# Kernel tuning notes

Hardware: AMD Instinct MI355X
Metric: run time of the kernel (lower is better)

The kernel has to match this reference:

```python
import jax, jax.numpy as jnp
import numpy as np

N, E, F, H, C, G = 50000, 800000, 20, 4, 64, 64
D = H * C           # 256 = hidden_dim * heads
OUT = 256
L = 6               # 3 res blocks x depth 2 GATv2 layers
NEG_SLOPE = 0.2     # PyG GATv2Conv default negative_slope


def setup_inputs() -> dict:
    key = jax.random.key(0)
    ks = jax.random.split(key, 16)
    def nrm(k, shape, fan_in):
        return jax.random.normal(k, shape, jnp.float32) * (1.0 / np.sqrt(fan_in))
    return {
        "x": jax.random.normal(ks[0], (N, F), jnp.float32),
        "pos": jax.random.normal(ks[1], (N, 3), jnp.float32) * 10.0,
        "edge_index": jax.random.randint(ks[2], (2, E), 0, N),
        "batch": jnp.sort(jax.random.randint(ks[3], (N,), 0, G)),
        # edge_MLP1 = MLP([1, 32, 1])
        "mlp_w1": nrm(ks[4], (1, 32), 1),
        "mlp_b1": jnp.zeros((32,), jnp.float32),
        "mlp_w2": nrm(ks[5], (32, 1), 32),
        "mlp_b2": jnp.zeros((1,), jnp.float32),
        "w_in": nrm(ks[6], (F, D), F),
        "b_in": jnp.zeros((D,), jnp.float32),
        # 6 stacked GATv2Conv layers (all in=D, heads=H, out-per-head=C)
        "gat_wl": nrm(ks[7], (L, D, D), D),
        "gat_bl": jnp.zeros((L, D), jnp.float32),
        "gat_wr": nrm(ks[8], (L, D, D), D),
        "gat_br": jnp.zeros((L, D), jnp.float32),
        "gat_we": nrm(ks[9], (L, 1, D), 1),      # lin_edge, edge_dim=1, no bias
        "gat_att": nrm(ks[10], (L, H, C), C),
        "gat_bias": jnp.zeros((L, D), jnp.float32),
        # 3 AttentionalAggregation modules: gate_nn=Linear(D,1), nn=Linear(D,D)
        "gate_w": nrm(ks[11], (3, D, 1), D),
        "gate_b": jnp.zeros((3, 1), jnp.float32),
        "nn_w": nrm(ks[12], (3, D, D), D),
        "nn_b": jnp.zeros((3, D), jnp.float32),
        "out_w1": nrm(ks[13], (3 * D, OUT), 3 * D),
        "out_b1": jnp.zeros((OUT,), jnp.float32),
        "out_w2": nrm(ks[14], (OUT, OUT), OUT),
        "out_b2": jnp.zeros((OUT,), jnp.float32),
    }


def _segment_softmax(logits, seg, num_segments):
    m = jax.ops.segment_max(logits, seg, num_segments=num_segments)
    e = jnp.exp(logits - m[seg])
    s = jax.ops.segment_sum(e, seg, num_segments=num_segments)
    return e / (s[seg] + 1e-16)


def _gatv2(h, src, dst, ew, wl, bl, wr, br, we, att, bias):
    # h: [N, D]; ew: [E, 1] edge features
    n = h.shape[0]
    xl = (h @ wl + bl).reshape(n, H, C)           # source-side transform (x_j)
    xr = (h @ wr + br).reshape(n, H, C)           # target-side transform (x_i)
    ee = (ew @ we).reshape(-1, H, C)              # edge transform (no bias)
    xj = xl[src]                                  # [E, H, C]
    g = jax.nn.leaky_relu(xj + xr[dst] + ee, NEG_SLOPE)
    alpha = jnp.einsum('ehc,hc->eh', g, att)      # [E, H]
    alpha = _segment_softmax(alpha, dst, n)       # softmax over incoming edges
    out = jax.ops.segment_sum(xj * alpha[:, :, None], dst, num_segments=n)
    return out.reshape(n, D) + bias


def _agg(h, batch, gw, gb, nw, nb):
    gate = _segment_softmax((h @ gw + gb)[:, 0], batch, G)     # [N]
    v = h @ nw + nb
    return jax.ops.segment_sum(gate[:, None] * v, batch, num_segments=G)


def _forward(x, pos, mlp_w1, mlp_b1, mlp_w2, mlp_b2, w_in, b_in,
             gat_wl, gat_bl, gat_wr, gat_br, gat_we, gat_att, gat_bias,
             gate_w, gate_b, nn_w, nn_b, out_w1, out_b1, out_w2, out_b2,
             edge_index, batch):
    src, dst = edge_index[0], edge_index[1]
    d = jnp.linalg.norm(pos[src] - pos[dst], axis=1)[:, None]          # [E,1]
    ew = jax.nn.relu(jax.nn.relu(d @ mlp_w1 + mlp_b1) @ mlp_w2 + mlp_b2)  # [E,1]
    h = x @ w_in + b_in                                                # [N,D]
    outs = []
    for blk in range(3):
        for j in range(2):
            i = blk * 2 + j
            h = h + _gatv2(h, src, dst, ew, gat_wl[i], gat_bl[i], gat_wr[i],
                           gat_br[i], gat_we[i], gat_att[i], gat_bias[i])
            h = jax.nn.relu(h)   # Dropout -> identity (eval mode)
        outs.append(_agg(h, batch, gate_w[blk], gate_b[blk], nn_w[blk], nn_b[blk]))
    z = jnp.concatenate(outs, axis=1)                                  # [G, 3D]
    enc = jax.nn.relu(z @ out_w1 + out_b1) @ out_w2 + out_b2
    return h, enc


def reference(x, pos, edge_index, batch, mlp_w1, mlp_b1, mlp_w2, mlp_b2,
              w_in, b_in, gat_wl, gat_bl, gat_wr, gat_br, gat_we, gat_att,
              gat_bias, gate_w, gate_b, nn_w, nn_b, out_w1, out_b1,
              out_w2, out_b2):
    return _forward(x, pos, mlp_w1, mlp_b1, mlp_w2, mlp_b2, w_in, b_in,
                    gat_wl, gat_bl, gat_wr, gat_br, gat_we, gat_att, gat_bias,
                    gate_w, gate_b, nn_w, nn_b, out_w1, out_b1, out_w2, out_b2,
                    edge_index, batch)
```

## Files before the change

kernel.cpp:

```cpp
#include <hip/hip_runtime.h>
#include <math.h>

constexpr int F_IN = 20;
constexpr int DDIM = 256;

typedef __attribute__((ext_vector_type(8))) short bf16x8;
typedef __attribute__((ext_vector_type(4))) float f32x4;

__device__ __forceinline__ float lrelu(float x){ return x > 0.f ? x : 0.2f*x; }

__device__ __forceinline__ float b2f(unsigned short u){
  union { unsigned int i; float f; } x; x.i = ((unsigned int)u) << 16; return x.f;
}
__device__ __forceinline__ unsigned short f2b(float f){
  union { float f; unsigned int i; } x; x.f = f;
  unsigned int r = x.i + 0x7fffu + ((x.i >> 16) & 1u);
  return (unsigned short)(r >> 16);
}

__global__ __launch_bounds__(256) void edge_prep_k(
    const int* __restrict__ ei, const float* __restrict__ pos,
    const float* __restrict__ mw1, const float* __restrict__ mb1,
    const float* __restrict__ mw2, const float* __restrict__ mb2,
    float* __restrict__ ew, int* __restrict__ cnt, int E)
{
  int t = blockIdx.x*256 + threadIdx.x;
  if (t >= E) return;
  int s = ei[t], d = ei[E + t];
  float dx = pos[s*3+0]-pos[d*3+0];
  float dy = pos[s*3+1]-pos[d*3+1];
  float dz = pos[s*3+2]-pos[d*3+2];
  float dist = sqrtf(dx*dx+dy*dy+dz*dz);
  float o = mb2[0];
  #pragma unroll
  for (int j=0;j<32;j++){
    float hj = fmaxf(dist*mw1[j]+mb1[j], 0.f);
    o += hj*mw2[j];
  }
  o = fmaxf(o, 0.f);
  ew[t] = o;
  atomicAdd(&cnt[d], 1);
}

__global__ __launch_bounds__(512) void scan1_k(const int* __restrict__ cnt, int* __restrict__ offs,
                                               int* __restrict__ bsum, int n)
{
  __shared__ int t[512];
  int tid = threadIdx.x;
  int i = blockIdx.x*512 + tid;
  int v = (i < n) ? cnt[i] : 0;
  t[tid] = v;
  __syncthreads();
  for (int s = 1; s < 512; s <<= 1) {
    int y = (tid >= s) ? t[tid - s] : 0;
    __syncthreads();
    if (tid >= s) t[tid] += y;
    __syncthreads();
  }
  if (i < n) offs[i] = t[tid] - v;
  if (tid == 511) bsum[blockIdx.x] = t[511];
}

__global__ __launch_bounds__(512) void scan2_k(const int* __restrict__ bsum, int* __restrict__ bpre, int nb)
{
  __shared__ int t[512];
  int tid = threadIdx.x;
  int v = (tid < nb) ? bsum[tid] : 0;
  t[tid] = v;
  __syncthreads();
  for (int s = 1; s < 512; s <<= 1) {
    int y = (tid >= s) ? t[tid - s] : 0;
    __syncthreads();
    if (tid >= s) t[tid] += y;
    __syncthreads();
  }
  bpre[tid] = t[tid] - v;
}

__global__ __launch_bounds__(512) void scan3_k(int* __restrict__ offs, const int* __restrict__ bpre, int n, int e)
{
  int i = blockIdx.x*512 + threadIdx.x;
  if (i < n) offs[i] += bpre[blockIdx.x];
  if (i == 0) offs[n] = e;
}

__global__ __launch_bounds__(256) void scatter_k(const int* __restrict__ ei, const float* __restrict__ ew,
    int* __restrict__ cur, int* __restrict__ ssrc, float* __restrict__ sew, int E)
{
  int t = blockIdx.x*256 + threadIdx.x;
  if (t >= E) return;
  int d = ei[E+t];
  int p = atomicAdd(&cur[d], 1);
  ssrc[p] = ei[t];
  sew[p] = ew[t];
}

__global__ void gseg_k(const int* __restrict__ batch, int* __restrict__ goff, int n){
  int g = threadIdx.x;
  if (g > 64) return;
  int lo = 0, hi = n;
  while (lo < hi){ int mid = (lo + hi) >> 1; if (batch[mid] < g) lo = mid + 1; else hi = mid; }
  goff[g] = lo;
}

__global__ __launch_bounds__(256) void wt_k(const float* __restrict__ gwl, const float* __restrict__ gwr,
                                            unsigned short* __restrict__ Wt)
{
  __shared__ float t[64][65];
  int ct = blockIdx.x;
  int kt = blockIdx.y;
  int layer = blockIdx.z;
  int tid = threadIdx.x;
  int cbase = ct*64, k0 = kt*64;
  const float* src = (cbase < 256) ? (gwl + (size_t)layer*65536) : (gwr + (size_t)layer*65536);
  int csrc0 = (cbase < 256) ? cbase : cbase - 256;
  #pragma unroll
  for (int j = 0; j < 16; ++j){
    int idx = j*256 + tid;
    int kl = idx >> 6, cl = idx & 63;
    t[cl][kl] = src[(size_t)(k0 + kl)*256 + csrc0 + cl];
  }
  __syncthreads();
  #pragma unroll
  for (int j = 0; j < 16; ++j){
    int idx = j*256 + tid;
    int cl = idx >> 6, kl = idx & 63;
    Wt[(size_t)layer*131072 + (size_t)(cbase + cl)*256 + k0 + kl] = f2b(t[cl][kl]);
  }
}

__global__ __launch_bounds__(256) void h0_k(const float* __restrict__ x, const float* __restrict__ w,
    const float* __restrict__ b, float* __restrict__ h, unsigned short* __restrict__ hb, int n)
{
  __shared__ float xs[16][20];
  int row0 = blockIdx.x*16, tid = threadIdx.x;
  for (int idx = tid; idx < 16*20; idx += 256){
    int r = idx/20, c = idx%20;
    int rr = row0 + r;
    xs[r][c] = (rr < n) ? x[rr*20 + c] : 0.f;
  }
  __syncthreads();
  float bj = b[tid];
  float acc[16];
  #pragma unroll
  for (int r=0;r<16;r++) acc[r] = bj;
  for (int k=0;k<20;k++){
    float wv = w[k*256 + tid];
    #pragma unroll
    for (int r=0;r<16;r++) acc[r] += xs[r][k]*wv;
  }
  #pragma unroll
  for (int r=0;r<16;r++){
    int rr = row0 + r;
    if (rr < n){
      h[(size_t)rr*256 + tid] = acc[r];
      hb[(size_t)rr*256 + tid] = f2b(acc[r]);
    }
  }
}

__global__ __launch_bounds__(256) void gemm_mfma_k(
    const unsigned short* __restrict__ hb,
    const unsigned short* __restrict__ Wt,
    const float* __restrict__ bl, const float* __restrict__ br,
    unsigned short* __restrict__ out,
    int n)
{
  __shared__ short As[128*64];
  __shared__ short Bs[128*64];
  int tid = threadIdx.x;
  int lane = tid & 63, wid = tid >> 6;
  int wr = wid >> 1, wc = wid & 1;
  int row0 = blockIdx.x * 128;
  int col0 = blockIdx.y * 128;
  f32x4 acc[4][4] = {};

  for (int k0 = 0; k0 < 256; k0 += 64) {
    #pragma unroll
    for (int j = 0; j < 4; ++j) {
      int c = j*256 + tid;
      int r = c >> 3, q = c & 7;
      int rg = row0 + r; if (rg > n-1) rg = n-1;
      bf16x8 av = *(const bf16x8*)(hb + (size_t)rg*256 + k0 + q*8);
      bf16x8 bv = *(const bf16x8*)(Wt + (size_t)(col0 + r)*256 + k0 + q*8);
      int qs = (q ^ (r & 7)) * 8;
      *(bf16x8*)(As + r*64 + qs) = av;
      *(bf16x8*)(Bs + r*64 + qs) = bv;
    }
    __syncthreads();
    #pragma unroll
    for (int kk = 0; kk < 2; ++kk) {
      bf16x8 a[4], b[4];
      #pragma unroll
      for (int mi = 0; mi < 4; ++mi) {
        int r = wr*64 + mi*16 + (lane & 15);
        int q = (kk*4 + (lane >> 4)) ^ (r & 7);
        a[mi] = *(const bf16x8*)(As + r*64 + q*8);
      }
      #pragma unroll
      for (int ni = 0; ni < 4; ++ni) {
        int r = wc*64 + ni*16 + (lane & 15);
        int q = (kk*4 + (lane >> 4)) ^ (r & 7);
        b[ni] = *(const bf16x8*)(Bs + r*64 + q*8);
      }
      #pragma unroll
      for (int mi = 0; mi < 4; ++mi)
        #pragma unroll
        for (int ni = 0; ni < 4; ++ni)
          acc[mi][ni] = __builtin_amdgcn_mfma_f32_16x16x32_bf16(a[mi], b[ni], acc[mi][ni], 0, 0, 0);
    }
    __syncthreads();
  }

  const float* bias = (col0 < 256) ? bl : br;
  int cb = (col0 < 256) ? col0 : col0 - 256;
  #pragma unroll
  for (int ni = 0; ni < 4; ++ni) {
    int coff = wc*64 + ni*16 + (lane & 15);
    int col = col0 + coff;
    float bv = bias[cb + coff];
    #pragma unroll
    for (int mi = 0; mi < 4; ++mi) {
      #pragma unroll
      for (int e = 0; e < 4; ++e) {
        int row = row0 + wr*64 + mi*16 + (lane >> 4)*4 + e;
        if (row < n) out[(size_t)row*512 + col] = f2b(acc[mi][ni][e] + bv);
      }
    }
  }
}

__global__ __launch_bounds__(256) void gat_agg_k(
    const unsigned short* __restrict__ xlr,
    const int* __restrict__ offs, const int* __restrict__ ssrc, const float* __restrict__ sew,
    const float* __restrict__ we, const float* __restrict__ att, const float* __restrict__ bias,
    float* __restrict__ h, unsigned short* __restrict__ hb, int n)
{
  int wid = blockIdx.x*4 + (threadIdx.x >> 6);
  if (wid >= n) return;
  int lane = threadIdx.x & 63;
  const ushort4* xv = (const ushort4*)xlr;
  ushort4 xru = xv[(size_t)wid*128 + 64 + lane];
  float xrx = b2f(xru.x), xry = b2f(xru.y), xrz = b2f(xru.z), xrw = b2f(xru.w);
  float4 we4 = ((const float4*)we)[lane];
  float4 at4 = ((const float4*)att)[lane];
  float m = -INFINITY, sden = 0.f;
  float ax=0.f, ay=0.f, az=0.f, aw=0.f;
  int k = offs[wid], kend = offs[wid+1];
  int src; float ewv; ushort4 xj;
  if (k < kend){ src = ssrc[k]; ewv = sew[k]; xj = xv[(size_t)src*128 + lane]; }
  while (k < kend){
    float cx = b2f(xj.x), cy = b2f(xj.y), cz = b2f(xj.z), cw = b2f(xj.w);
    float ce = ewv;
    ++k;
    if (k < kend){ src = ssrc[k]; ewv = sew[k]; xj = xv[(size_t)src*128 + lane]; }
    float gx = lrelu(cx + xrx + ce*we4.x);
    float gy = lrelu(cy + xry + ce*we4.y);
    float gz = lrelu(cz + xrz + ce*we4.z);
    float gw_ = lrelu(cw + xrw + ce*we4.w);
    float p = gx*at4.x + gy*at4.y + gz*at4.z + gw_*at4.w;
    p += __shfl_xor(p, 1);
    p += __shfl_xor(p, 2);
    p += __shfl_xor(p, 4);
    p += __shfl_xor(p, 8);
    float mn = fmaxf(m, p);
    float corr = __expf(m - mn);
    float wv = __expf(p - mn);
    sden = sden*corr + wv;
    ax = ax*corr + wv*cx;
    ay = ay*corr + wv*cy;
    az = az*corr + wv*cz;
    aw = aw*corr + wv*cw;
    m = mn;
  }
  float inv = 1.f/(sden + 1e-16f);
  size_t hi = (size_t)wid*64 + lane;
  float4 hv = ((const float4*)h)[hi];
  float4 b4 = ((const float4*)bias)[lane];
  float4 o;
  o.x = fmaxf(hv.x + ax*inv + b4.x, 0.f);
  o.y = fmaxf(hv.y + ay*inv + b4.y, 0.f);
  o.z = fmaxf(hv.z + az*inv + b4.z, 0.f);
  o.w = fmaxf(hv.w + aw*inv + b4.w, 0.f);
  ((float4*)h)[hi] = o;
  ushort4 ob;
  ob.x = f2b(o.x); ob.y = f2b(o.y); ob.z = f2b(o.z); ob.w = f2b(o.w);
  ((ushort4*)hb)[hi] = ob;
}

__global__ __launch_bounds__(256) void logits_k(const float* __restrict__ h, const float* __restrict__ gw,
    const float* __restrict__ gb, float* __restrict__ logit, int n)
{
  int wid = blockIdx.x*4 + (threadIdx.x >> 6);
  if (wid >= n) return;
  int lane = threadIdx.x & 63;
  float4 hv = ((const float4*)h)[(size_t)wid*64 + lane];
  float4 g4 = ((const float4*)gw)[lane];
  float p = hv.x*g4.x + hv.y*g4.y + hv.z*g4.z + hv.w*g4.w;
  #pragma unroll
  for (int s=1; s<64; s<<=1) p += __shfl_xor(p, s);
  if (lane == 0) logit[wid] = p + gb[0];
}

__global__ __launch_bounds__(1024) void pool_k(const float* __restrict__ h, const float* __restrict__ logit,
    const int* __restrict__ goff, float* __restrict__ hbar)
{
  __shared__ float red[1024];
  __shared__ float mS, sS;
  int g = blockIdx.x, tid = threadIdx.x;
  int b0 = goff[g], b1 = goff[g+1];
  float lm = -INFINITY;
  for (int i = b0 + tid; i < b1; i += 1024) lm = fmaxf(lm, logit[i]);
  red[tid] = lm;
  __syncthreads();
  for (int s = 512; s > 0; s >>= 1){
    if (tid < s) red[tid] = fmaxf(red[tid], red[tid+s]);
    __syncthreads();
  }
  if (tid == 0) mS = red[0];
  __syncthreads();
  float m = mS;
  float sw = 0.f;
  for (int i = b0 + tid; i < b1; i += 1024) sw += __expf(logit[i] - m);
  __syncthreads();
  red[tid] = sw;
  __syncthreads();
  for (int s = 512; s > 0; s >>= 1){
    if (tid < s) red[tid] += red[tid+s];
    __syncthreads();
  }
  if (tid == 0) sS = red[0];
  __syncthreads();
  float sden = sS;
  int ch = tid & 255, rs = tid >> 8;
  float acc = 0.f;
  for (int i = b0 + rs; i < b1; i += 4)
    acc += __expf(logit[i] - m) * h[(size_t)i*256 + ch];
  __syncthreads();
  red[tid] = acc;
  __syncthreads();
  if (rs == 0){
    float a = red[ch] + red[256+ch] + red[512+ch] + red[768+ch];
    hbar[g*256 + ch] = a/(sden + 1e-16f);
  }
}

template<int K, bool RELU>
__global__ __launch_bounds__(256) void rowgemm_k(const float* __restrict__ A, const float* __restrict__ W,
    const float* __restrict__ bias, float* __restrict__ out, int ostride)
{
  __shared__ float ar[K];
  int row = blockIdx.x;
  int tid = threadIdx.x;
  for (int i = tid; i < K; i += 256) ar[i] = A[(size_t)row*K + i];
  __syncthreads();
  float acc = bias[tid];
  for (int k = 0; k < K; ++k) acc += ar[k]*W[k*256 + tid];
  if (RELU) acc = fmaxf(acc, 0.f);
  out[(size_t)row*ostride + tid] = acc;
}

extern "C" void kernel_launch(void* const* d_in, const int* in_sizes, int n_in,
                              void* d_out, int out_size, void* d_ws, size_t ws_size,
                              hipStream_t stream)
{
  const float* x     = (const float*)d_in[0];
  const float* pos   = (const float*)d_in[1];
  const int*   ei    = (const int*)d_in[2];
  const int*   batch = (const int*)d_in[3];
  const float* mw1   = (const float*)d_in[4];
  const float* mb1   = (const float*)d_in[5];
  const float* mw2   = (const float*)d_in[6];
  const float* mb2   = (const float*)d_in[7];
  const float* w_in  = (const float*)d_in[8];
  const float* b_in  = (const float*)d_in[9];
  const float* gwl   = (const float*)d_in[10];
  const float* gbl   = (const float*)d_in[11];
  const float* gwr   = (const float*)d_in[12];
  const float* gbr   = (const float*)d_in[13];
  const float* gwe   = (const float*)d_in[14];
  const float* gatt  = (const float*)d_in[15];
  const float* gbias = (const float*)d_in[16];
  const float* gate_w= (const float*)d_in[17];
  const float* gate_b= (const float*)d_in[18];
  const float* nn_w  = (const float*)d_in[19];
  const float* nn_b  = (const float*)d_in[20];
  const float* ow1   = (const float*)d_in[21];
  const float* ob1   = (const float*)d_in[22];
  const float* ow2   = (const float*)d_in[23];
  const float* ob2   = (const float*)d_in[24];

  const int N = in_sizes[0] / F_IN;
  const int E = in_sizes[2] / 2;

  char* ws = (char*)d_ws;
  size_t woff = 0;
  auto alloc = [&](size_t bytes) -> void* {
    void* p = ws + woff;
    woff = (woff + bytes + 255) & ~(size_t)255;
    return p;
  };
  float* ew    = (float*)alloc((size_t)E*4);
  int*   cnt   = (int*)  alloc((size_t)N*4);
  int*   offs  = (int*)  alloc((size_t)(N+1)*4);
  int*   cur   = (int*)  alloc((size_t)N*4);
  int*   bsum  = (int*)  alloc(512*4);
  int*   bpre  = (int*)  alloc(512*4);
  int*   ssrc  = (int*)  alloc((size_t)E*4);
  float* sew   = (float*)alloc((size_t)E*4);
  float* h     = (float*)alloc((size_t)N*DDIM*4);
  unsigned short* hb  = (unsigned short*)alloc((size_t)N*DDIM*2);
  unsigned short* xlr = (unsigned short*)alloc((size_t)N*512*2);
  unsigned short* Wt  = (unsigned short*)alloc((size_t)6*512*256*2);
  float* logit = (float*)alloc((size_t)N*4);
  int*   goff  = (int*)  alloc(68*4);
  float* hbar  = (float*)alloc(64*DDIM*4);
  float* zcat  = (float*)alloc(64*768*4);
  float* t1    = (float*)alloc(64*DDIM*4);
  (void)ws_size; (void)n_in; (void)out_size;

  hipMemsetAsync(cnt, 0, (size_t)N*4, stream);

  int eb = (E + 255)/256;
  edge_prep_k<<<eb, 256, 0, stream>>>(ei, pos, mw1, mb1, mw2, mb2, ew, cnt, E);
  int nb = (N + 511)/512;
  scan1_k<<<nb, 512, 0, stream>>>(cnt, offs, bsum, N);
  scan2_k<<<1, 512, 0, stream>>>(bsum, bpre, nb);
  scan3_k<<<nb, 512, 0, stream>>>(offs, bpre, N, E);
  hipMemcpyAsync(cur, offs, (size_t)N*4, hipMemcpyDeviceToDevice, stream);
  scatter_k<<<eb, 256, 0, stream>>>(ei, ew, cur, ssrc, sew, E);

  gseg_k<<<1, 128, 0, stream>>>(batch, goff, N);
  wt_k<<<dim3(8,4,6), 256, 0, stream>>>(gwl, gwr, Wt);

  h0_k<<<(N + 15)/16, 256, 0, stream>>>(x, w_in, b_in, h, hb, N);

  int gx = (N + 127)/128;
  int wavegrid = (N + 3)/4;
  for (int i = 0; i < 6; ++i) {
    gemm_mfma_k<<<dim3(gx, 4), 256, 0, stream>>>(hb, Wt + (size_t)i*131072,
        gbl + i*256, gbr + i*256, xlr, N);
    gat_agg_k<<<wavegrid, 256, 0, stream>>>(xlr, offs, ssrc, sew,
        gwe + i*256, gatt + i*256, gbias + i*256, h, hb, N);
    if (i & 1) {
      int blk = i >> 1;
      logits_k<<<wavegrid, 256, 0, stream>>>(h, gate_w + blk*256, gate_b + blk, logit, N);
      pool_k<<<64, 1024, 0, stream>>>(h, logit, goff, hbar);
      rowgemm_k<256,false><<<64, 256, 0, stream>>>(hbar, nn_w + (size_t)blk*65536,
          nn_b + blk*256, zcat + blk*256, 768);
    }
  }
  rowgemm_k<768,true><<<64, 256, 0, stream>>>(zcat, ow1, ob1, t1, 256);
  rowgemm_k<256,false><<<64, 256, 0, stream>>>(t1, ow2, ob2, (float*)d_out + (size_t)N*DDIM, 256);
  hipMemcpyAsync(d_out, h, (size_t)N*DDIM*4, hipMemcpyDeviceToDevice, stream);
}
```

Before: 1.368 ms.

## Process four edges per wave in GAT aggregation with lazy softmax rescaling

```diff
diff --git a/kernel.cpp b/kernel.cpp
--- a/kernel.cpp
+++ b/kernel.cpp
@@ -234,58 +234,116 @@
     const unsigned short* __restrict__ xlr,
     const int* __restrict__ offs, const int* __restrict__ ssrc, const float* __restrict__ sew,
     const float* __restrict__ we, const float* __restrict__ att, const float* __restrict__ bias,
-    float* __restrict__ h, unsigned short* __restrict__ hb, int n)
+    float* __restrict__ h, unsigned short* __restrict__ hb, float* __restrict__ hout, int n)
 {
   int wid = blockIdx.x*4 + (threadIdx.x >> 6);
   if (wid >= n) return;
   int lane = threadIdx.x & 63;
-  const ushort4* xv = (const ushort4*)xlr;
-  ushort4 xru = xv[(size_t)wid*128 + 64 + lane];
-  float xrx = b2f(xru.x), xry = b2f(xru.y), xrz = b2f(xru.z), xrw = b2f(xru.w);
-  float4 we4 = ((const float4*)we)[lane];
-  float4 at4 = ((const float4*)att)[lane];
-  float m = -INFINITY, sden = 0.f;
-  float ax=0.f, ay=0.f, az=0.f, aw=0.f;
-  int k = offs[wid], kend = offs[wid+1];
-  int src; float ewv; ushort4 xj;
-  if (k < kend){ src = ssrc[k]; ewv = sew[k]; xj = xv[(size_t)src*128 + lane]; }
-  while (k < kend){
-    float cx = b2f(xj.x), cy = b2f(xj.y), cz = b2f(xj.z), cw = b2f(xj.w);
-    float ce = ewv;
-    ++k;
-    if (k < kend){ src = ssrc[k]; ewv = sew[k]; xj = xv[(size_t)src*128 + lane]; }
-    float gx = lrelu(cx + xrx + ce*we4.x);
-    float gy = lrelu(cy + xry + ce*we4.y);
-    float gz = lrelu(cz + xrz + ce*we4.z);
-    float gw_ = lrelu(cw + xrw + ce*we4.w);
-    float p = gx*at4.x + gy*at4.y + gz*at4.z + gw_*at4.w;
+  int g = lane >> 4, l = lane & 15;
+  int c0 = l*16;
+
+  float xr[16], wef[16], atf[16];
+  {
+    const unsigned short* xrp = xlr + (size_t)wid*512 + 256 + c0;
+    bf16x8 r0 = *(const bf16x8*)xrp;
+    bf16x8 r1 = *(const bf16x8*)(xrp + 8);
+    #pragma unroll
+    for (int i=0;i<8;i++){ xr[i] = b2f((unsigned short)r0[i]); xr[8+i] = b2f((unsigned short)r1[i]); }
+    #pragma unroll
+    for (int q=0;q<4;q++){
+      float4 wv = *(const float4*)(we + c0 + q*4);
+      float4 av = *(const float4*)(att + c0 + q*4);
+      wef[q*4+0]=wv.x; wef[q*4+1]=wv.y; wef[q*4+2]=wv.z; wef[q*4+3]=wv.w;
+      atf[q*4+0]=av.x; atf[q*4+1]=av.y; atf[q*4+2]=av.z; atf[q*4+3]=av.w;
+    }
+  }
+
+  float m = -1e30f, s = 0.f;
+  float a[16];
+  #pragma unroll
+  for (int i=0;i<16;i++) a[i] = 0.f;
+
+  int k = offs[wid] + g, kend = offs[wid+1];
+  int src; float ewv = 0.f;
+  bf16x8 xa = {0,0,0,0,0,0,0,0};
+  bf16x8 xb = {0,0,0,0,0,0,0,0};
+  if (k < kend){
+    src = ssrc[k]; ewv = sew[k];
+    const unsigned short* xp = xlr + (size_t)src*512 + c0;
+    xa = *(const bf16x8*)xp; xb = *(const bf16x8*)(xp + 8);
+  }
+  while (__any(k < kend)) {
+    bool act = (k < kend);
+    bf16x8 ca = xa, cb = xb; float ce = ewv;
+    k += 4;
+    if (k < kend){
+      src = ssrc[k]; ewv = sew[k];
+      const unsigned short* xp = xlr + (size_t)src*512 + c0;
+      xa = *(const bf16x8*)xp; xb = *(const bf16x8*)(xp + 8);
+    }
+    float xjf[16];
+    #pragma unroll
+    for (int i=0;i<8;i++){ xjf[i] = b2f((unsigned short)ca[i]); xjf[8+i] = b2f((unsigned short)cb[i]); }
+    float p = 0.f;
+    #pragma unroll
+    for (int i=0;i<16;i++){
+      float t = fmaf(ce, wef[i], xjf[i] + xr[i]);
+      t = fmaxf(t, 0.2f*t);
+      p = fmaf(t, atf[i], p);
+    }
     p += __shfl_xor(p, 1);
     p += __shfl_xor(p, 2);
-    p += __shfl_xor(p, 4);
-    p += __shfl_xor(p, 8);
-    float mn = fmaxf(m, p);
-    float corr = __expf(m - mn);
-    float wv = __expf(p - mn);
-    sden = sden*corr + wv;
-    ax = ax*corr + wv*cx;
-    ay = ay*corr + wv*cy;
-    az = az*corr + wv*cz;
-    aw = aw*corr + wv*cw;
+    if (!act) p = -1e30f;
+    if (__any(p > m + 8.f)) {
+      float mn = fmaxf(m, p);
+      float corr = __expf(m - mn);
+      float wv = act ? __expf(p - mn) : 0.f;
+      s = s*corr + wv;
+      #pragma unroll
+      for (int i=0;i<16;i++) a[i] = fmaf(a[i], corr, wv*xjf[i]);
+      m = mn;
+    } else {
+      float wv = act ? __expf(p - m) : 0.f;
+      s += wv;
+      #pragma unroll
+      for (int i=0;i<16;i++) a[i] = fmaf(wv, xjf[i], a[i]);
+    }
+  }
+
+  #pragma unroll
+  for (int d = 16; d <= 32; d <<= 1) {
+    float mo = __shfl_xor(m, d);
+    float so = __shfl_xor(s, d);
+    float mn = fmaxf(m, mo);
+    float cs = __expf(m - mn), co = __expf(mo - mn);
+    s = s*cs + so*co;
+    #pragma unroll
+    for (int i=0;i<16;i++){
+      float ao = __shfl_xor(a[i], d);
+      a[i] = fmaf(a[i], cs, ao*co);
+    }
     m = mn;
   }
-  float inv = 1.f/(sden + 1e-16f);
-  size_t hi = (size_t)wid*64 + lane;
-  float4 hv = ((const float4*)h)[hi];
-  float4 b4 = ((const float4*)bias)[lane];
-  float4 o;
-  o.x = fmaxf(hv.x + ax*inv + b4.x, 0.f);
-  o.y = fmaxf(hv.y + ay*inv + b4.y, 0.f);
-  o.z = fmaxf(hv.z + az*inv + b4.z, 0.f);
-  o.w = fmaxf(hv.w + aw*inv + b4.w, 0.f);
-  ((float4*)h)[hi] = o;
-  ushort4 ob;
-  ob.x = f2b(o.x); ob.y = f2b(o.y); ob.z = f2b(o.z); ob.w = f2b(o.w);
-  ((ushort4*)hb)[hi] = ob;
+
+  if (g == 0) {
+    float inv = 1.f/(s + 1e-16f);
+    size_t base = (size_t)wid*256 + c0;
+    #pragma unroll
+    for (int q = 0; q < 4; ++q) {
+      float4 hv = *(const float4*)(h + base + q*4);
+      float4 b4 = *(const float4*)(bias + c0 + q*4);
+      float4 o;
+      o.x = fmaxf(hv.x + a[q*4+0]*inv + b4.x, 0.f);
+      o.y = fmaxf(hv.y + a[q*4+1]*inv + b4.y, 0.f);
+      o.z = fmaxf(hv.z + a[q*4+2]*inv + b4.z, 0.f);
+      o.w = fmaxf(hv.w + a[q*4+3]*inv + b4.w, 0.f);
+      *(float4*)(h + base + q*4) = o;
+      ushort4 ob;
+      ob.x = f2b(o.x); ob.y = f2b(o.y); ob.z = f2b(o.z); ob.w = f2b(o.w);
+      *(ushort4*)(hb + base + q*4) = ob;
+      if (hout) *(float4*)(hout + base + q*4) = o;
+    }
+  }
 }
 
 __global__ __launch_bounds__(256) void logits_k(const float* __restrict__ h, const float* __restrict__ gw,
@@ -440,8 +498,9 @@
   for (int i = 0; i < 6; ++i) {
     gemm_mfma_k<<<dim3(gx, 4), 256, 0, stream>>>(hb, Wt + (size_t)i*131072,
         gbl + i*256, gbr + i*256, xlr, N);
+    float* hout = (i == 5) ? (float*)d_out : (float*)nullptr;
     gat_agg_k<<<wavegrid, 256, 0, stream>>>(xlr, offs, ssrc, sew,
-        gwe + i*256, gatt + i*256, gbias + i*256, h, hb, N);
+        gwe + i*256, gatt + i*256, gbias + i*256, h, hb, hout, N);
     if (i & 1) {
       int blk = i >> 1;
       logits_k<<<wavegrid, 256, 0, stream>>>(h, gate_w + blk*256, gate_b + blk, logit, N);
@@ -452,5 +511,4 @@
   }
   rowgemm_k<768,true><<<64, 256, 0, stream>>>(zcat, ow1, ob1, t1, 256);
   rowgemm_k<256,false><<<64, 256, 0, stream>>>(t1, ow2, ob2, (float*)d_out + (size_t)N*DDIM, 256);
-  hipMemcpyAsync(d_out, h, (size_t)N*DDIM*4, hipMemcpyDeviceToDevice, stream);
-}
+}
```

After: 1.408 ms. +2.9%, slower.
